# Optimization experiments

Hardware: AMD Instinct MI355X
Metric: run time of the kernel (lower is better)

The kernel has to match this reference:

```python
import jax, jax.numpy as jnp
import numpy as np

B, C, T, H, W, E, K = 2, 256, 16, 32, 32, 4, 2


def setup_inputs() -> dict:
    key = jax.random.key(0)
    ks = jax.random.split(key, 5)
    x = jax.random.normal(ks[0], (B, C, T, H, W), dtype=jnp.float32)
    # gate: Conv3d(dim, E, 1) -> weight [E, C], bias [E]
    gate_w = jax.random.normal(ks[1], (E, C), dtype=jnp.float32) * 0.02
    gate_b = jnp.zeros((E,), dtype=jnp.float32)
    # experts_layer1: Conv3d(dim, dim*E, 1) -> weight [E*C, C], bias [E*C]
    w1 = jax.random.normal(ks[2], (E * C, C), dtype=jnp.float32) * 0.02
    b1 = jnp.zeros((E * C,), dtype=jnp.float32)
    # experts_layer2: Conv3d(dim*E, dim*E, 1, groups=E) -> per-expert [C, C]
    w2 = jax.random.normal(ks[3], (E, C, C), dtype=jnp.float32) * 0.02
    b2 = jnp.zeros((E, C), dtype=jnp.float32)
    return {"x": x, "gate_w": gate_w, "gate_b": gate_b,
            "w1": w1, "b1": b1, "w2": w2, "b2": b2}


def reference(x, gate_w, gate_b, w1, b1, w2, b2):
    # gating: 1x1x1 conv == channel contraction; logits [B,T,H,W,E]
    logits = jnp.einsum('bcthw,ec->bthwe', x, gate_w) + gate_b
    vals, idx = jax.lax.top_k(logits, K)              # [B,T,H,W,K]
    wk = jax.nn.softmax(vals, axis=-1).astype(x.dtype)
    # scatter top-k softmax weights back into E slots (zeros elsewhere)
    weights = jnp.sum(jax.nn.one_hot(idx, E, dtype=x.dtype) * wk[..., None],
                      axis=-2)                        # [B,T,H,W,E]
    # layer1 (dense 1x1x1 conv) + SiLU; output channels = E*C
    h = jax.nn.silu(jnp.einsum('bcthw,oc->bothw', x, w1)
                    + b1[None, :, None, None, None])
    h = h.reshape(B, E, C, T, H, W)
    # layer2: grouped 1x1x1 conv, one [C,C] matmul per expert
    expert_out = (jnp.einsum('becthw,eoc->beothw', h, w2)
                  + b2[None, :, :, None, None, None])  # [B,E,C,T,H,W]
    # weighted combine over experts + residual
    out = jnp.einsum('becthw,bthwe->bcthw', expert_out, weights)
    return out + x
```

## Files before the change

### kernel.cpp

```cpp
#include <hip/hip_runtime.h>
#include <hip/hip_bf16.h>


#define C_DIM 256
#define S_DIM 16384
#define E_DIM 4
#define MT 64
#define XST 264
#define OST 68
#define WFRAG_ELEMS 262144

typedef __attribute__((ext_vector_type(8))) short bf16x8;
typedef __attribute__((ext_vector_type(4))) float f32x4;

__device__ __forceinline__ short bfq(float f) {
  __hip_bfloat16 h = __float2bfloat16(f);
  return *(short*)&h;
}

__global__ __launch_bounds__(256) void prepack_kernel(
    const float* __restrict__ w1, const float* __restrict__ w2,
    __hip_bfloat16* __restrict__ dst)
{
  int o8 = blockIdx.x * 256 + threadIdx.x;
  int o  = o8 << 3;
  int half = o >> 18;
  int idx  = o & (WFRAG_ELEMS - 1);
  int lane = (idx >> 3) & 63;
  int kc   = (idx >> 9) & 7;
  int nt   = (idx >> 12) & 15;
  int e    = (idx >> 16) & 3;
  const float* src = half ? w2 : w1;
  const float* s = src + (e*256 + nt*16 + (lane & 15))*256 + kc*32 + (lane >> 4)*8;
  const float4 v0 = *(const float4*)s;
  const float4 v1 = *(const float4*)(s + 4);
  bf16x8 outv = {bfq(v0.x), bfq(v0.y), bfq(v0.z), bfq(v0.w),
                 bfq(v1.x), bfq(v1.y), bfq(v1.z), bfq(v1.w)};
  *(bf16x8*)((short*)dst + o) = outv;
}

template<int MTC>
__device__ __forceinline__ void gemm1_sparse(
    const short* XsS, short* HsS, const short* w1e, const float* b1e,
    const unsigned char* plist_e, const float* wgtg_e,
    int wv, int r, int q, bool dosync)
{
  f32x4 hacc[MTC][2];
#pragma unroll
  for (int i = 0; i < MTC; ++i)
#pragma unroll
    for (int j = 0; j < 2; ++j) hacc[i][j] = (f32x4){0.f, 0.f, 0.f, 0.f};

  int aoff[MTC];
#pragma unroll
  for (int Mt = 0; Mt < MTC; ++Mt)
    aoff[Mt] = (int)plist_e[Mt*16 + r] * XST;

  bf16x8 bw[2][2];
#pragma unroll
  for (int t = 0; t < 2; ++t) bw[0][t] = *(const bf16x8*)(w1e + (t*8 + 0)*512);
#pragma unroll
  for (int kc = 0; kc < 8; ++kc) {
    if (kc < 7) {
#pragma unroll
      for (int t = 0; t < 2; ++t)
        bw[(kc+1)&1][t] = *(const bf16x8*)(w1e + (t*8 + kc + 1)*512);
    }
    bf16x8 a[MTC];
#pragma unroll
    for (int Mt = 0; Mt < MTC; ++Mt)
      a[Mt] = *(const bf16x8*)(XsS + aoff[Mt] + kc*32 + q*8);
#pragma unroll
    for (int Mt = 0; Mt < MTC; ++Mt)
#pragma unroll
      for (int t = 0; t < 2; ++t)
        hacc[Mt][t] = __builtin_amdgcn_mfma_f32_16x16x32_bf16(a[Mt], bw[kc&1][t], hacc[Mt][t], 0, 0, 0);
  }

  if (dosync) __syncthreads();

#pragma unroll
  for (int Mt = 0; Mt < MTC; ++Mt) {
    const int g0 = Mt*16 + q*4;
    const unsigned pw = *(const unsigned*)(plist_e + g0);
    const f32x4 wg = *(const f32x4*)(wgtg_e + g0);
#pragma unroll
    for (int t = 0; t < 2; ++t) {
      const int n = wv*32 + t*16 + r;
      const float bias = b1e[n];
#pragma unroll
      for (int reg = 0; reg < 4; ++reg) {
        const int p = (pw >> (8*reg)) & 255;
        const float z = hacc[Mt][t][reg] + bias;
        const float s = __builtin_amdgcn_rcpf(1.0f + __expf(-z));
        HsS[p*XST + n] = bfq(z * s * wg[reg]);
      }
    }
  }
}

__global__ __launch_bounds__(512, 4) void moe_fused_kernel(
    const float* __restrict__ x,
    const float* __restrict__ gate_w,
    const float* __restrict__ gate_b,
    const float* __restrict__ b1,
    const float* __restrict__ b2,
    const __hip_bfloat16* __restrict__ wp,
    float* __restrict__ out)
{
  __shared__ __align__(16) char pool[256 * OST * 4];
  __shared__ __align__(16) float Wgt[MT * 4];
  __shared__ __align__(16) unsigned char plist[4][64];
  __shared__ __align__(16) float WgtG[4][64];
  __shared__ __align__(4)  unsigned char zlist[4][64];
  __shared__ int mcnt[4];

  short* XsS = (short*)pool;
  short* HsS = (short*)(pool + MT * XST * 2);
  float* Os  = (float*)pool;

  const int tid  = threadIdx.x;
  const int lane = tid & 63;
  const int wv   = tid >> 6;
  const int r    = lane & 15;
  const int q    = lane >> 4;

  const int g  = blockIdx.x;
  const int b  = g >> 8;
  const int s0 = (g & 255) * MT;
  const float* xb = x + (size_t)b * C_DIM * S_DIM + s0;

  {
    const int p  = lane;
    const int c0 = wv * 32;
    float xv[32];
#pragma unroll
    for (int j = 0; j < 32; ++j)
      xv[j] = xb[(size_t)(c0 + j) * S_DIM + p];

    double acc[4] = {0.0, 0.0, 0.0, 0.0};
#pragma unroll
    for (int j = 0; j < 32; ++j) {
      const double xd = (double)xv[j];
      acc[0] += xd * (double)gate_w[0*256 + c0 + j];
      acc[1] += xd * (double)gate_w[1*256 + c0 + j];
      acc[2] += xd * (double)gate_w[2*256 + c0 + j];
      acc[3] += xd * (double)gate_w[3*256 + c0 + j];
    }

#pragma unroll
    for (int k = 0; k < 4; ++k) {
      bf16x8 blk = {bfq(xv[k*8+0]), bfq(xv[k*8+1]), bfq(xv[k*8+2]), bfq(xv[k*8+3]),
                    bfq(xv[k*8+4]), bfq(xv[k*8+5]), bfq(xv[k*8+6]), bfq(xv[k*8+7])};
      *(bf16x8*)(XsS + p*XST + c0 + k*8) = blk;
    }

    double* GateD = (double*)HsS;
#pragma unroll
    for (int e = 0; e < 4; ++e)
      GateD[(e*8 + wv)*64 + p] = acc[e];
  }
  __syncthreads();

  if (tid < 256) {
    const int p = tid >> 2;
    const int e = tid & 3;
    const double* GateD = (const double*)HsS;
    double s = (double)gate_b[e];
#pragma unroll
    for (int g2 = 0; g2 < 8; ++g2) s += GateD[(e*8 + g2)*64 + p];
    const float la = (float)s;
    const float lb = __shfl_xor(la, 1, 64);
    const float lc = __shfl_xor(la, 2, 64);
    const float ld = __shfl_xor(lb, 2, 64);
    if (e == 0) {
      const float l0 = la, l1 = lb, l2 = lc, l3 = ld;
      int i1 = 0; float v1 = l0;
      if (l1 > v1) { v1 = l1; i1 = 1; }
      if (l2 > v1) { v1 = l2; i1 = 2; }
      if (l3 > v1) { v1 = l3; i1 = 3; }
      float v2 = -3.0e38f; int i2 = 0;
      if (i1 != 0 && l0 > v2) { v2 = l0; i2 = 0; }
      if (i1 != 1 && l1 > v2) { v2 = l1; i2 = 1; }
      if (i1 != 2 && l2 > v2) { v2 = l2; i2 = 2; }
      if (i1 != 3 && l3 > v2) { v2 = l3; i2 = 3; }
      const float wA = 1.0f / (1.0f + __expf(v2 - v1));
      const float wB = 1.0f - wA;
      f32x4 w;
      w[0] = (i1 == 0) ? wA : ((i2 == 0) ? wB : 0.0f);
      w[1] = (i1 == 1) ? wA : ((i2 == 1) ? wB : 0.0f);
      w[2] = (i1 == 2) ? wA : ((i2 == 2) ? wB : 0.0f);
      w[3] = (i1 == 3) ? wA : ((i2 == 3) ? wB : 0.0f);
      *(f32x4*)(&Wgt[p*4]) = w;
    }
  }
  __syncthreads();

  if (wv < 4) {
    const int e = wv;
    const int p = lane;
    const float w = Wgt[p*4 + e];
    const bool sel = (w != 0.0f);
    const unsigned long long mask = __ballot(sel);
    const int below = __popcll(mask & ((1ull << p) - 1ull));
    const int m = __popcll(mask);
    const int pad = (((m + 15) >> 4) << 4) - m;
    if (sel) {
      plist[e][below] = (unsigned char)p;
      WgtG[e][below]  = w;
    } else {
      const int zidx = p - below;
      zlist[e][zidx] = (unsigned char)p;
      if (zidx < pad) {
        plist[e][m + zidx] = (unsigned char)p;
        WgtG[e][m + zidx]  = 0.0f;
      }
    }
    if (p == 0) mcnt[e] = m;
  }
  __syncthreads();

  const short* W1P = (const short*)wp;
  const short* W2P = (const short*)wp + WFRAG_ELEMS;

  f32x4 oacc[4][2];
#pragma unroll
  for (int i = 0; i < 4; ++i)
#pragma unroll
    for (int j = 0; j < 2; ++j) oacc[i][j] = (f32x4){0.f, 0.f, 0.f, 0.f};

  for (int e = 0; e < E_DIM; ++e) {
    const int me = mcnt[e];
    const int mt = __builtin_amdgcn_readfirstlane((me + 15) >> 4);
    const short* w1e = W1P + ((e*16 + wv*2)*8)*512 + lane*8;
    const float* b1e = b1 + e*256;
    const bool dosync = (e > 0);

    if      (mt == 2) gemm1_sparse<2>(XsS, HsS, w1e, b1e, plist[e], WgtG[e], wv, r, q, dosync);
    else if (mt == 3) gemm1_sparse<3>(XsS, HsS, w1e, b1e, plist[e], WgtG[e], wv, r, q, dosync);
    else if (mt == 4) gemm1_sparse<4>(XsS, HsS, w1e, b1e, plist[e], WgtG[e], wv, r, q, dosync);
    else if (mt == 1) gemm1_sparse<1>(XsS, HsS, w1e, b1e, plist[e], WgtG[e], wv, r, q, dosync);
    else { if (dosync) __syncthreads(); }

    const short* w2e = W2P + ((e*16 + wv*2)*8)*512 + lane*8;
    bf16x8 cw[2][2];
#pragma unroll
    for (int t = 0; t < 2; ++t) cw[0][t] = *(const bf16x8*)(w2e + (t*8 + 0)*512);

    {
      const int zm = 64 - me;
      const bf16x8 zz = {0,0,0,0,0,0,0,0};
      for (int i = tid; i < zm*32; i += 512) {
        const int row = zlist[e][i >> 5];
        *(bf16x8*)(HsS + row*XST + (i & 31)*8) = zz;
      }
    }
    __syncthreads();

    {
#pragma unroll
      for (int kc = 0; kc < 8; ++kc) {
        if (kc < 7) {
#pragma unroll
          for (int t = 0; t < 2; ++t)
            cw[(kc+1)&1][t] = *(const bf16x8*)(w2e + (t*8 + kc + 1)*512);
        }
        bf16x8 a[4];
#pragma unroll
        for (int Mt = 0; Mt < 4; ++Mt)
          a[Mt] = *(const bf16x8*)(HsS + (Mt*16 + r)*XST + kc*32 + q*8);
#pragma unroll
        for (int Mt = 0; Mt < 4; ++Mt)
#pragma unroll
          for (int t = 0; t < 2; ++t)
            oacc[Mt][t] = __builtin_amdgcn_mfma_f32_16x16x32_bf16(a[Mt], cw[kc&1][t], oacc[Mt][t], 0, 0, 0);
      }
    }
  }
  __syncthreads();

  {
    float b2v[2][4];
#pragma unroll
    for (int t = 0; t < 2; ++t) {
      const int c = wv*32 + t*16 + r;
#pragma unroll
      for (int e = 0; e < 4; ++e) b2v[t][e] = b2[e*256 + c];
    }
#pragma unroll
    for (int Mt = 0; Mt < 4; ++Mt) {
      f32x4 wv4[4];
#pragma unroll
      for (int reg = 0; reg < 4; ++reg)
        wv4[reg] = *(const f32x4*)(&Wgt[(Mt*16 + q*4 + reg)*4]);
#pragma unroll
      for (int t = 0; t < 2; ++t) {
        f32x4 v = oacc[Mt][t];
#pragma unroll
        for (int reg = 0; reg < 4; ++reg)
          v[reg] += wv4[reg][0]*b2v[t][0] + wv4[reg][1]*b2v[t][1]
                  + wv4[reg][2]*b2v[t][2] + wv4[reg][3]*b2v[t][3];
        *(f32x4*)(Os + (size_t)(wv*32 + t*16 + r)*OST + Mt*16 + q*4) = v;
      }
    }
  }
  __syncthreads();

  {
    const int p4 = (tid & 15) * 4;
    const int cg = tid >> 4;
    float* ob = out + (size_t)b * C_DIM * S_DIM + s0;
#pragma unroll
    for (int cc = 0; cc < 8; ++cc) {
      const int c = cc*32 + cg;
      const f32x4  o  = *(const f32x4*)(Os + (size_t)c*OST + p4);
      const float4 xr = *(const float4*)(xb + (size_t)c*S_DIM + p4);
      float4 res;
      res.x = o[0] + xr.x; res.y = o[1] + xr.y;
      res.z = o[2] + xr.z; res.w = o[3] + xr.w;
      *(float4*)(ob + (size_t)c*S_DIM + p4) = res;
    }
  }
}

extern "C" void kernel_launch(void* const* d_in, const int* in_sizes, int n_in,
                              void* d_out, int out_size, void* d_ws, size_t ws_size,
                              hipStream_t stream)
{
  (void)in_sizes; (void)n_in; (void)out_size; (void)ws_size;
  const float* x      = (const float*)d_in[0];
  const float* gate_w = (const float*)d_in[1];
  const float* gate_b = (const float*)d_in[2];
  const float* w1     = (const float*)d_in[3];
  const float* b1     = (const float*)d_in[4];
  const float* w2     = (const float*)d_in[5];
  const float* b2     = (const float*)d_in[6];
  float* out = (float*)d_out;
  __hip_bfloat16* wpack = (__hip_bfloat16*)d_ws;

  prepack_kernel<<<256, 256, 0, stream>>>(w1, w2, wpack);
  moe_fused_kernel<<<512, 512, 0, stream>>>(x, gate_w, gate_b, b1, b2, wpack, out);
}
```

Baseline: 126.4 us.

## Write epilogue directly from accumulators, add MFMA priority, coalesce prepack reads

The epilogue now adds the residual and stores to global memory straight from the MFMA accumulators, which drops the LDS staging buffer and its two barriers. LDS use shrinks to the X/H tiles. s_setprio raises wave priority around the MFMA loops, and the prepack kernel is remapped so each thread reads consecutive source rows while scattering to the fragment layout. The direct stores write 16-byte chunks per lane with a channel stride, which may coalesce worse than the old staged row-contiguous writes.

```diff
diff --git a/kernel.cpp b/kernel.cpp
--- a/kernel.cpp
+++ b/kernel.cpp
@@ -7,7 +7,6 @@
 #define E_DIM 4
 #define MT 64
 #define XST 264
-#define OST 68
 #define WFRAG_ELEMS 262144
 
 typedef __attribute__((ext_vector_type(8))) short bf16x8;
@@ -22,21 +21,25 @@
     const float* __restrict__ w1, const float* __restrict__ w2,
     __hip_bfloat16* __restrict__ dst)
 {
-  int o8 = blockIdx.x * 256 + threadIdx.x;
-  int o  = o8 << 3;
-  int half = o >> 18;
-  int idx  = o & (WFRAG_ELEMS - 1);
-  int lane = (idx >> 3) & 63;
-  int kc   = (idx >> 9) & 7;
-  int nt   = (idx >> 12) & 15;
-  int e    = (idx >> 16) & 3;
+  int o8   = blockIdx.x * 256 + threadIdx.x;
+  int half = o8 >> 15;
+  int idx  = o8 & 32767;
+  int j    = idx & 31;
+  int rowid= idx >> 5;
+  int e    = rowid >> 8;
+  int nt   = (rowid >> 4) & 15;
+  int row  = rowid & 15;
+  int kc   = j >> 2;
+  int col8 = j & 3;
+  int lane = (col8 << 4) | row;
   const float* src = half ? w2 : w1;
-  const float* s = src + (e*256 + nt*16 + (lane & 15))*256 + kc*32 + (lane >> 4)*8;
+  const float* s = src + rowid * 256 + j * 8;
   const float4 v0 = *(const float4*)s;
   const float4 v1 = *(const float4*)(s + 4);
   bf16x8 outv = {bfq(v0.x), bfq(v0.y), bfq(v0.z), bfq(v0.w),
                  bfq(v1.x), bfq(v1.y), bfq(v1.z), bfq(v1.w)};
-  *(bf16x8*)((short*)dst + o) = outv;
+  int chunk = ((e*16 + nt)*8 + kc)*64 + lane;
+  *(bf16x8*)((short*)dst + half*WFRAG_ELEMS + chunk*8) = outv;
 }
 
 template<int MTC>
@@ -59,6 +62,7 @@
   bf16x8 bw[2][2];
 #pragma unroll
   for (int t = 0; t < 2; ++t) bw[0][t] = *(const bf16x8*)(w1e + (t*8 + 0)*512);
+  __builtin_amdgcn_s_setprio(1);
 #pragma unroll
   for (int kc = 0; kc < 8; ++kc) {
     if (kc < 7) {
@@ -76,6 +80,7 @@
       for (int t = 0; t < 2; ++t)
         hacc[Mt][t] = __builtin_amdgcn_mfma_f32_16x16x32_bf16(a[Mt], bw[kc&1][t], hacc[Mt][t], 0, 0, 0);
   }
+  __builtin_amdgcn_s_setprio(0);
 
   if (dosync) __syncthreads();
 
@@ -108,7 +113,7 @@
     const __hip_bfloat16* __restrict__ wp,
     float* __restrict__ out)
 {
-  __shared__ __align__(16) char pool[256 * OST * 4];
+  __shared__ __align__(16) char pool[2 * MT * XST * 2];
   __shared__ __align__(16) float Wgt[MT * 4];
   __shared__ __align__(16) unsigned char plist[4][64];
   __shared__ __align__(16) float WgtG[4][64];
@@ -117,7 +122,6 @@
 
   short* XsS = (short*)pool;
   short* HsS = (short*)(pool + MT * XST * 2);
-  float* Os  = (float*)pool;
 
   const int tid  = threadIdx.x;
   const int lane = tid & 63;
@@ -129,6 +133,9 @@
   const int b  = g >> 8;
   const int s0 = (g & 255) * MT;
   const float* xb = x + (size_t)b * C_DIM * S_DIM + s0;
+
+  const short* W1P = (const short*)wp;
+  const short* W2P = (const short*)wp + WFRAG_ELEMS;
 
   {
     const int p  = lane;
@@ -220,9 +227,6 @@
   }
   __syncthreads();
 
-  const short* W1P = (const short*)wp;
-  const short* W2P = (const short*)wp + WFRAG_ELEMS;
-
   f32x4 oacc[4][2];
 #pragma unroll
   for (int i = 0; i < 4; ++i)
@@ -248,7 +252,7 @@
     for (int t = 0; t < 2; ++t) cw[0][t] = *(const bf16x8*)(w2e + (t*8 + 0)*512);
 
     {
-      const int zm = 64 - me;
+      const int zm = MT - me;
       const bf16x8 zz = {0,0,0,0,0,0,0,0};
       for (int i = tid; i < zm*32; i += 512) {
         const int row = zlist[e][i >> 5];
@@ -258,6 +262,7 @@
     __syncthreads();
 
     {
+      __builtin_amdgcn_s_setprio(1);
 #pragma unroll
       for (int kc = 0; kc < 8; ++kc) {
         if (kc < 7) {
@@ -275,9 +280,9 @@
           for (int t = 0; t < 2; ++t)
             oacc[Mt][t] = __builtin_amdgcn_mfma_f32_16x16x32_bf16(a[Mt], cw[kc&1][t], oacc[Mt][t], 0, 0, 0);
       }
-    }
-  }
-  __syncthreads();
+      __builtin_amdgcn_s_setprio(0);
+    }
+  }
 
   {
     float b2v[2][4];
@@ -287,38 +292,28 @@
 #pragma unroll
       for (int e = 0; e < 4; ++e) b2v[t][e] = b2[e*256 + c];
     }
+    float* ob = out + (size_t)b * C_DIM * S_DIM + s0;
 #pragma unroll
     for (int Mt = 0; Mt < 4; ++Mt) {
+      const int pb = Mt*16 + q*4;
       f32x4 wv4[4];
 #pragma unroll
       for (int reg = 0; reg < 4; ++reg)
-        wv4[reg] = *(const f32x4*)(&Wgt[(Mt*16 + q*4 + reg)*4]);
+        wv4[reg] = *(const f32x4*)(&Wgt[(pb + reg)*4]);
 #pragma unroll
       for (int t = 0; t < 2; ++t) {
+        const int c = wv*32 + t*16 + r;
         f32x4 v = oacc[Mt][t];
 #pragma unroll
         for (int reg = 0; reg < 4; ++reg)
           v[reg] += wv4[reg][0]*b2v[t][0] + wv4[reg][1]*b2v[t][1]
                   + wv4[reg][2]*b2v[t][2] + wv4[reg][3]*b2v[t][3];
-        *(f32x4*)(Os + (size_t)(wv*32 + t*16 + r)*OST + Mt*16 + q*4) = v;
-      }
-    }
-  }
-  __syncthreads();
-
-  {
-    const int p4 = (tid & 15) * 4;
-    const int cg = tid >> 4;
-    float* ob = out + (size_t)b * C_DIM * S_DIM + s0;
-#pragma unroll
-    for (int cc = 0; cc < 8; ++cc) {
-      const int c = cc*32 + cg;
-      const f32x4  o  = *(const f32x4*)(Os + (size_t)c*OST + p4);
-      const float4 xr = *(const float4*)(xb + (size_t)c*S_DIM + p4);
-      float4 res;
-      res.x = o[0] + xr.x; res.y = o[1] + xr.y;
-      res.z = o[2] + xr.z; res.w = o[3] + xr.w;
-      *(float4*)(ob + (size_t)c*S_DIM + p4) = res;
+        const float4 xr = *(const float4*)(xb + (size_t)c*S_DIM + pb);
+        float4 res;
+        res.x = v[0] + xr.x; res.y = v[1] + xr.y;
+        res.z = v[2] + xr.z; res.w = v[3] + xr.w;
+        *(float4*)(ob + (size_t)c*S_DIM + pb) = res;
+      }
     }
   }
 }
```

After: 128.7 us. No clear change (+1.8%).
